# Performance work log

Hardware: AMD Instinct MI355X
Metric: run time of the kernel (lower is better)

Reference implementation:

```python
import jax, jax.numpy as jnp
import numpy as np

B, S, D = 32, 2048, 64

def setup_inputs() -> dict:
    key = jax.random.key(0)
    kq, kk, kv = jax.random.split(key, 3)
    return {
        "query": jax.random.normal(kq, (B, S, D), dtype=jnp.float32),
        "key": jax.random.normal(kk, (B, S, D), dtype=jnp.float32),
        "value": jax.random.normal(kv, (B, S, D), dtype=jnp.float32),
    }

def reference(query, key, value):
    # scores: [B, S, S] = Q @ K^T / sqrt(d_k)  (scale=True)
    d_k = key.shape[-1]
    scores = jnp.einsum("bqd,bkd->bqk", query, key) / jnp.sqrt(jnp.asarray(d_k, query.dtype))
    # exp + normalize over last dim == softmax (no mask, dropout in eval mode)
    attn = jax.nn.softmax(scores, axis=-1)
    # context: [B, S, D] = attn @ V
    context = jnp.einsum("bqk,bkd->bqd", attn, value)
    return context
```

## Files before the change

kernel.cpp:

```cpp
#include <hip/hip_runtime.h>
#include <hip/hip_bf16.h>

#define B_   32
#define S_   2048
#define D_   64
#define KVB  64
#define NT   (S_/KVB)
#define NW   4
#define QW   64
#define QB   (NW*QW)

typedef __attribute__((ext_vector_type(8)))  __bf16 bf16x8;
typedef __attribute__((ext_vector_type(4)))  __bf16 bf16x4;
typedef __attribute__((ext_vector_type(16))) float  f32x16;

__device__ __forceinline__ float fexp2(float x) {
#if __has_builtin(__builtin_amdgcn_exp2f)
    return __builtin_amdgcn_exp2f(x);
#else
    return exp2f(x);
#endif
}

__device__ __forceinline__ unsigned pk2(float a, float b) {
    unsigned r;
    asm("v_cvt_pk_bf16_f32 %0, %1, %2" : "=v"(r) : "v"(a), "v"(b));
    return r;
}

__device__ __forceinline__ void pl32swap(unsigned &a, unsigned &b) {
#if __has_builtin(__builtin_amdgcn_permlane32_swap)
    auto r = __builtin_amdgcn_permlane32_swap(a, b, false, false);
    a = (unsigned)r[0]; b = (unsigned)r[1];
#else
    unsigned pa = (unsigned)__shfl_xor((int)a, 32);
    unsigned pb = (unsigned)__shfl_xor((int)b, 32);
    bool hi = (threadIdx.x & 32) != 0;
    unsigned na = hi ? pb : a;
    unsigned nb = hi ? b  : pa;
    a = na; b = nb;
#endif
}

__device__ __forceinline__ f32x16 z16() {
    f32x16 z;
    #pragma unroll
    for (int i = 0; i < 16; ++i) z[i] = 0.f;
    return z;
}

struct PBpair { bf16x8 a, b; };

__device__ __forceinline__ PBpair pack2(const f32x16 ps) {
    unsigned y0 = pk2(ps[0],  ps[1]);
    unsigned y1 = pk2(ps[2],  ps[3]);
    unsigned y2 = pk2(ps[4],  ps[5]);
    unsigned y3 = pk2(ps[6],  ps[7]);
    pl32swap(y0, y2); pl32swap(y1, y3);
    unsigned z0 = pk2(ps[8],  ps[9]);
    unsigned z1 = pk2(ps[10], ps[11]);
    unsigned z2 = pk2(ps[12], ps[13]);
    unsigned z3 = pk2(ps[14], ps[15]);
    pl32swap(z0, z2); pl32swap(z1, z3);
    union { unsigned u[4]; bf16x8 v; } pa, pbu;
    pa.u[0]=y0;  pa.u[1]=y1;  pa.u[2]=y2;  pa.u[3]=y3;
    pbu.u[0]=z0; pbu.u[1]=z1; pbu.u[2]=z2; pbu.u[3]=z3;
    PBpair r; r.a = pa.v; r.b = pbu.v; return r;
}

__global__ __launch_bounds__(256, 1)
void attn_fwd(const float* __restrict__ Q, const float* __restrict__ K,
              const float* __restrict__ V, float* __restrict__ Out)
{
    __shared__ __align__(16) __bf16 Kt[3][KVB * D_];
    __shared__ __align__(16) __bf16 Vt[3][D_ * KVB];

    const int tid  = threadIdx.x;
    const int w    = tid >> 6;
    const int lane = tid & 63;
    const int l31  = lane & 31;
    const int hi   = lane >> 5;

    const int bid = blockIdx.x;
    const int swz = ((bid & 7) << 5) | (bid >> 3);
    const int b   = swz >> 3;
    const int q0  = (swz & 7) * QB;

    const float SCL = 0.18033688011112042f;
    bf16x8 qfA[4], qfB[4];
    #pragma unroll
    for (int qt = 0; qt < 2; ++qt) {
        const float* qp = Q + ((size_t)(b*S_ + q0 + w*QW + qt*32 + l31))*D_ + hi*8;
        #pragma unroll
        for (int ks = 0; ks < 4; ++ks) {
            float4 f0 = *reinterpret_cast<const float4*>(qp + ks*16);
            float4 f1 = *reinterpret_cast<const float4*>(qp + ks*16 + 4);
            bf16x8 a;
            a[0]=(__bf16)(f0.x*SCL); a[1]=(__bf16)(f0.y*SCL);
            a[2]=(__bf16)(f0.z*SCL); a[3]=(__bf16)(f0.w*SCL);
            a[4]=(__bf16)(f1.x*SCL); a[5]=(__bf16)(f1.y*SCL);
            a[6]=(__bf16)(f1.z*SCL); a[7]=(__bf16)(f1.w*SCL);
            if (qt == 0) qfA[ks]=a; else qfB[ks]=a;
        }
    }

    int offK[4], offV[4];
    #pragma unroll
    for (int i = 0; i < 4; ++i) {
        offK[i] = l31*128 + (((i*32) + hi*16) ^ ((l31 & 7) << 4));
        offV[i] = l31*128 + (((i*32) + hi*16) ^ (((l31 >> 1) & 7) << 4));
    }

    const float* kg = K + (size_t)b*S_*D_;
    const float* vg = V + (size_t)b*S_*D_;

    const int krow0 = tid >> 4;
    const int kcol  = (tid & 15) * 4;
    const int kwr0  = krow0*128 + ((kcol*2) ^ ((krow0 & 7) << 4));

    const int kv0 = (tid >> 4) * 2;
    const int db  = (tid & 15) * 2;
    int vwr[4];
    #pragma unroll
    for (int j = 0; j < 4; ++j) {
        int d = db + (j >> 1)*32 + (j & 1);
        vwr[j] = d*128 + ((kv0*2) ^ (((d >> 1) & 7) << 4));
    }

#define STAGE_LOAD(T)                                                              \
    {   const float* kt_ = kg + (size_t)(T)*KVB*D_;                                \
        const float* vt_ = vg + (size_t)(T)*KVB*D_;                                \
        ka0 = *reinterpret_cast<const float4*>(kt_ + krow0*64 + kcol);             \
        ka1 = *reinterpret_cast<const float4*>(kt_ + (krow0+16)*64 + kcol);        \
        ka2 = *reinterpret_cast<const float4*>(kt_ + (krow0+32)*64 + kcol);        \
        ka3 = *reinterpret_cast<const float4*>(kt_ + (krow0+48)*64 + kcol);        \
        v0a = *reinterpret_cast<const float2*>(vt_ + kv0*64 + db);                 \
        v1a = *reinterpret_cast<const float2*>(vt_ + (kv0+1)*64 + db);             \
        v0b = *reinterpret_cast<const float2*>(vt_ + kv0*64 + db + 32);            \
        v1b = *reinterpret_cast<const float2*>(vt_ + (kv0+1)*64 + db + 32);        \
        v2a = *reinterpret_cast<const float2*>(vt_ + (kv0+32)*64 + db);            \
        v3a = *reinterpret_cast<const float2*>(vt_ + (kv0+33)*64 + db);            \
        v2b = *reinterpret_cast<const float2*>(vt_ + (kv0+32)*64 + db + 32);       \
        v3b = *reinterpret_cast<const float2*>(vt_ + (kv0+33)*64 + db + 32);       }

#define STAGE_WRITE(BUF)                                                           \
    {   char* kw = (char*)&Kt[(BUF)][0];                                           \
        char* vw = (char*)&Vt[(BUF)][0];                                           \
        bf16x4 h0 = {(__bf16)ka0.x,(__bf16)ka0.y,(__bf16)ka0.z,(__bf16)ka0.w};     \
        bf16x4 h1 = {(__bf16)ka1.x,(__bf16)ka1.y,(__bf16)ka1.z,(__bf16)ka1.w};     \
        bf16x4 h2 = {(__bf16)ka2.x,(__bf16)ka2.y,(__bf16)ka2.z,(__bf16)ka2.w};     \
        bf16x4 h3 = {(__bf16)ka3.x,(__bf16)ka3.y,(__bf16)ka3.z,(__bf16)ka3.w};     \
        *reinterpret_cast<bf16x4*>(kw + kwr0)        = h0;                         \
        *reinterpret_cast<bf16x4*>(kw + kwr0 + 2048) = h1;                         \
        *reinterpret_cast<bf16x4*>(kw + kwr0 + 4096) = h2;                         \
        *reinterpret_cast<bf16x4*>(kw + kwr0 + 6144) = h3;                         \
        *reinterpret_cast<unsigned*>(vw + vwr[0])        = pk2(v0a.x, v1a.x);      \
        *reinterpret_cast<unsigned*>(vw + vwr[1])        = pk2(v0a.y, v1a.y);      \
        *reinterpret_cast<unsigned*>(vw + vwr[2])        = pk2(v0b.x, v1b.x);      \
        *reinterpret_cast<unsigned*>(vw + vwr[3])        = pk2(v0b.y, v1b.y);      \
        *reinterpret_cast<unsigned*>(vw + (vwr[0] ^ 64)) = pk2(v2a.x, v3a.x);      \
        *reinterpret_cast<unsigned*>(vw + (vwr[1] ^ 64)) = pk2(v2a.y, v3a.y);      \
        *reinterpret_cast<unsigned*>(vw + (vwr[2] ^ 64)) = pk2(v2b.x, v3b.x);      \
        *reinterpret_cast<unsigned*>(vw + (vwr[3] ^ 64)) = pk2(v2b.y, v3b.y);      }

    float4 ka0, ka1, ka2, ka3;
    float2 v0a, v1a, v0b, v1b, v2a, v3a, v2b, v3b;

    STAGE_LOAD(0)
    STAGE_WRITE(0)
    __syncthreads();

    float lA = 0.f, lB = 0.f;
    f32x16 oA0 = z16(), oA1 = z16(), oB0 = z16(), oB1 = z16();
    PBpair pA01, pA23, pB01, pB23;

#define SOFTMAX_PACK()                                                             \
    {   _Pragma("unroll")                                                          \
        for (int r = 0; r < 16; ++r) sA0[r] = fexp2(sA0[r]);                       \
        _Pragma("unroll")                                                          \
        for (int r = 0; r < 16; ++r) sA1[r] = fexp2(sA1[r]);                       \
        _Pragma("unroll")                                                          \
        for (int r = 0; r < 16; ++r) sB0[r] = fexp2(sB0[r]);                       \
        _Pragma("unroll")                                                          \
        for (int r = 0; r < 16; ++r) sB1[r] = fexp2(sB1[r]);                       \
        float tA[16], tB[16];                                                      \
        _Pragma("unroll")                                                          \
        for (int i = 0; i < 16; ++i) { tA[i] = sA0[i] + sA1[i];                    \
                                       tB[i] = sB0[i] + sB1[i]; }                  \
        _Pragma("unroll")                                                          \
        for (int st = 8; st > 0; st >>= 1)                                         \
            _Pragma("unroll")                                                      \
            for (int i = 0; i < st; ++i) { tA[i] += tA[i+st]; tB[i] += tB[i+st]; } \
        lA += tA[0] + __shfl_xor(tA[0], 32);                                       \
        lB += tB[0] + __shfl_xor(tB[0], 32);                                       \
        pA01 = pack2(sA0); pA23 = pack2(sA1);                                      \
        pB01 = pack2(sB0); pB23 = pack2(sB1);                                      }

#define QK_BOTH(KBUF)                                                              \
    {   const char* kbuf = (const char*)&Kt[(KBUF)][0];                            \
        __builtin_amdgcn_s_setprio(1);                                             \
        _Pragma("unroll")                                                          \
        for (int ks = 0; ks < 4; ++ks) {                                           \
            bf16x8 k0 = *reinterpret_cast<const bf16x8*>(kbuf + offK[ks]);         \
            bf16x8 k1 = *reinterpret_cast<const bf16x8*>(kbuf + offK[ks] + 4096);  \
            sA0 = __builtin_amdgcn_mfma_f32_32x32x16_bf16(k0, qfA[ks], sA0, 0,0,0);\
            sB0 = __builtin_amdgcn_mfma_f32_32x32x16_bf16(k0, qfB[ks], sB0, 0,0,0);\
            sA1 = __builtin_amdgcn_mfma_f32_32x32x16_bf16(k1, qfA[ks], sA1, 0,0,0);\
            sB1 = __builtin_amdgcn_mfma_f32_32x32x16_bf16(k1, qfB[ks], sB1, 0,0,0);\
        }                                                                          \
        __builtin_amdgcn_s_setprio(0);                                             }

#define PV_BOTH(VBUF)                                                              \
    {   const char* vbuf = (const char*)&Vt[(VBUF)][0];                            \
        __builtin_amdgcn_s_setprio(1);                                             \
        _Pragma("unroll")                                                          \
        for (int c = 0; c < 4; ++c) {                                              \
            bf16x8 pa = (c==0)?pA01.a:(c==1)?pA01.b:(c==2)?pA23.a:pA23.b;          \
            bf16x8 pb = (c==0)?pB01.a:(c==1)?pB01.b:(c==2)?pB23.a:pB23.b;          \
            bf16x8 v0 = *reinterpret_cast<const bf16x8*>(vbuf + offV[c]);          \
            bf16x8 v1 = *reinterpret_cast<const bf16x8*>(vbuf + offV[c] + 4096);   \
            oA0 = __builtin_amdgcn_mfma_f32_32x32x16_bf16(v0, pa, oA0, 0,0,0);     \
            oB0 = __builtin_amdgcn_mfma_f32_32x32x16_bf16(v0, pb, oB0, 0,0,0);     \
            oA1 = __builtin_amdgcn_mfma_f32_32x32x16_bf16(v1, pa, oA1, 0,0,0);     \
            oB1 = __builtin_amdgcn_mfma_f32_32x32x16_bf16(v1, pb, oB1, 0,0,0);     \
        }                                                                          \
        __builtin_amdgcn_s_setprio(0);                                             }

    {
        STAGE_LOAD(1)
        f32x16 sA0 = z16(), sA1 = z16(), sB0 = z16(), sB1 = z16();
        QK_BOTH(0)
        SOFTMAX_PACK()
        STAGE_WRITE(1)
        __syncthreads();
    }

    for (int t = 1; t < NT; ++t) {
        const int cur = t % 3;
        const int prv = (t-1) % 3;
        const int nxt = (t+1) % 3;
        const int tn  = (t+1 < NT) ? (t+1) : t;
        STAGE_LOAD(tn)

        f32x16 sA0 = z16(), sA1 = z16(), sB0 = z16(), sB1 = z16();
        QK_BOTH(cur)
        PV_BOTH(prv)
        SOFTMAX_PACK()

        STAGE_WRITE(nxt)
        __syncthreads();
    }

    PV_BOTH((NT-1) % 3)

    {
        float invl = 1.0f / lA;
        float* orow = Out + ((size_t)(b*S_ + q0 + w*QW + l31))*D_;
        #pragma unroll
        for (int rr = 0; rr < 4; ++rr) {
            float4 res;
            res.x = oA0[rr*4+0]*invl; res.y = oA0[rr*4+1]*invl;
            res.z = oA0[rr*4+2]*invl; res.w = oA0[rr*4+3]*invl;
            *reinterpret_cast<float4*>(orow + rr*8 + hi*4) = res;
        }
        #pragma unroll
        for (int rr = 0; rr < 4; ++rr) {
            float4 res;
            res.x = oA1[rr*4+0]*invl; res.y = oA1[rr*4+1]*invl;
            res.z = oA1[rr*4+2]*invl; res.w = oA1[rr*4+3]*invl;
            *reinterpret_cast<float4*>(orow + 32 + rr*8 + hi*4) = res;
        }
    }
    {
        float invl = 1.0f / lB;
        float* orow = Out + ((size_t)(b*S_ + q0 + w*QW + 32 + l31))*D_;
        #pragma unroll
        for (int rr = 0; rr < 4; ++rr) {
            float4 res;
            res.x = oB0[rr*4+0]*invl; res.y = oB0[rr*4+1]*invl;
            res.z = oB0[rr*4+2]*invl; res.w = oB0[rr*4+3]*invl;
            *reinterpret_cast<float4*>(orow + rr*8 + hi*4) = res;
        }
        #pragma unroll
        for (int rr = 0; rr < 4; ++rr) {
            float4 res;
            res.x = oB1[rr*4+0]*invl; res.y = oB1[rr*4+1]*invl;
            res.z = oB1[rr*4+2]*invl; res.w = oB1[rr*4+3]*invl;
            *reinterpret_cast<float4*>(orow + 32 + rr*8 + hi*4) = res;
        }
    }
}

extern "C" void kernel_launch(void* const* d_in, const int* in_sizes, int n_in,
                              void* d_out, int out_size, void* d_ws, size_t ws_size,
                              hipStream_t stream) {
    const float* Q = (const float*)d_in[0];
    const float* K = (const float*)d_in[1];
    const float* V = (const float*)d_in[2];
    float* O = (float*)d_out;
    attn_fwd<<<dim3(B_ * (S_ / QB)), dim3(256), 0, stream>>>(Q, K, V, O);
}
```

Baseline: 62.46 us.

## Split KV sequence across two wave groups per block and merge partial outputs

Doubles the block to 512 threads (8 waves), where two groups of four waves each process half of every 128-row KV step for the same 256 queries, so the loop runs half as many iterations per wave. Partial O accumulators and row sums from group 1 are merged into group 0 through shared memory, reusing the K buffer, before normalization. The first QK MFMA now takes a zero accumulator instead of a zero-initialized register. The change raises per-CU wave count and latency hiding, at the cost of double the LDS staging, extra syncs and an LDS reduction epilogue.

```diff
diff --git a/kernel.cpp b/kernel.cpp
--- a/kernel.cpp
+++ b/kernel.cpp
@@ -5,10 +5,8 @@
 #define S_   2048
 #define D_   64
 #define KVB  64
-#define NT   (S_/KVB)
-#define NW   4
-#define QW   64
-#define QB   (NW*QW)
+#define NP   16
+#define QB   256
 
 typedef __attribute__((ext_vector_type(8)))  __bf16 bf16x8;
 typedef __attribute__((ext_vector_type(4)))  __bf16 bf16x4;
@@ -40,13 +38,6 @@
     unsigned nb = hi ? b  : pa;
     a = na; b = nb;
 #endif
-}
-
-__device__ __forceinline__ f32x16 z16() {
-    f32x16 z;
-    #pragma unroll
-    for (int i = 0; i < 16; ++i) z[i] = 0.f;
-    return z;
 }
 
 struct PBpair { bf16x8 a, b; };
@@ -68,18 +59,20 @@
     PBpair r; r.a = pa.v; r.b = pbu.v; return r;
 }
 
-__global__ __launch_bounds__(256, 1)
+__global__ __launch_bounds__(512, 2)
 void attn_fwd(const float* __restrict__ Q, const float* __restrict__ K,
               const float* __restrict__ V, float* __restrict__ Out)
 {
-    __shared__ __align__(16) __bf16 Kt[3][KVB * D_];
-    __shared__ __align__(16) __bf16 Vt[3][D_ * KVB];
+    __shared__ __align__(16) __bf16 Kt[3][2][KVB * D_];
+    __shared__ __align__(16) __bf16 Vt[3][2][D_ * KVB];
 
     const int tid  = threadIdx.x;
     const int w    = tid >> 6;
     const int lane = tid & 63;
     const int l31  = lane & 31;
     const int hi   = lane >> 5;
+    const int g2   = w >> 2;
+    const int qsub = w & 3;
 
     const int bid = blockIdx.x;
     const int swz = ((bid & 7) << 5) | (bid >> 3);
@@ -90,7 +83,7 @@
     bf16x8 qfA[4], qfB[4];
     #pragma unroll
     for (int qt = 0; qt < 2; ++qt) {
-        const float* qp = Q + ((size_t)(b*S_ + q0 + w*QW + qt*32 + l31))*D_ + hi*8;
+        const float* qp = Q + ((size_t)(b*S_ + q0 + qsub*64 + qt*32 + l31))*D_ + hi*8;
         #pragma unroll
         for (int ks = 0; ks < 4; ++ks) {
             float4 f0 = *reinterpret_cast<const float4*>(qp + ks*16);
@@ -114,12 +107,15 @@
     const float* kg = K + (size_t)b*S_*D_;
     const float* vg = V + (size_t)b*S_*D_;
 
-    const int krow0 = tid >> 4;
-    const int kcol  = (tid & 15) * 4;
+    const int ts   = tid >> 8;
+    const int t256 = tid & 255;
+
+    const int krow0 = t256 >> 4;
+    const int kcol  = (t256 & 15) * 4;
     const int kwr0  = krow0*128 + ((kcol*2) ^ ((krow0 & 7) << 4));
 
-    const int kv0 = (tid >> 4) * 2;
-    const int db  = (tid & 15) * 2;
+    const int kv0 = (t256 >> 4) * 2;
+    const int db  = (t256 & 15) * 2;
     int vwr[4];
     #pragma unroll
     for (int j = 0; j < 4; ++j) {
@@ -127,9 +123,9 @@
         vwr[j] = d*128 + ((kv0*2) ^ (((d >> 1) & 7) << 4));
     }
 
-#define STAGE_LOAD(T)                                                              \
-    {   const float* kt_ = kg + (size_t)(T)*KVB*D_;                                \
-        const float* vt_ = vg + (size_t)(T)*KVB*D_;                                \
+#define STAGE_LOAD(P)                                                              \
+    {   const float* kt_ = kg + ((size_t)(P)*128 + ts*64)*64;                      \
+        const float* vt_ = vg + ((size_t)(P)*128 + ts*64)*64;                      \
         ka0 = *reinterpret_cast<const float4*>(kt_ + krow0*64 + kcol);             \
         ka1 = *reinterpret_cast<const float4*>(kt_ + (krow0+16)*64 + kcol);        \
         ka2 = *reinterpret_cast<const float4*>(kt_ + (krow0+32)*64 + kcol);        \
@@ -144,8 +140,8 @@
         v3b = *reinterpret_cast<const float2*>(vt_ + (kv0+33)*64 + db + 32);       }
 
 #define STAGE_WRITE(BUF)                                                           \
-    {   char* kw = (char*)&Kt[(BUF)][0];                                           \
-        char* vw = (char*)&Vt[(BUF)][0];                                           \
+    {   char* kw = (char*)&Kt[(BUF)][ts][0];                                       \
+        char* vw = (char*)&Vt[(BUF)][ts][0];                                       \
         bf16x4 h0 = {(__bf16)ka0.x,(__bf16)ka0.y,(__bf16)ka0.z,(__bf16)ka0.w};     \
         bf16x4 h1 = {(__bf16)ka1.x,(__bf16)ka1.y,(__bf16)ka1.z,(__bf16)ka1.w};     \
         bf16x4 h2 = {(__bf16)ka2.x,(__bf16)ka2.y,(__bf16)ka2.z,(__bf16)ka2.w};     \
@@ -166,41 +162,26 @@
     float4 ka0, ka1, ka2, ka3;
     float2 v0a, v1a, v0b, v1b, v2a, v3a, v2b, v3b;
 
-    STAGE_LOAD(0)
-    STAGE_WRITE(0)
-    __syncthreads();
+    f32x16 ZV;
+    #pragma unroll
+    for (int i = 0; i < 16; ++i) ZV[i] = 0.f;
 
     float lA = 0.f, lB = 0.f;
-    f32x16 oA0 = z16(), oA1 = z16(), oB0 = z16(), oB1 = z16();
+    f32x16 oA0 = ZV, oA1 = ZV, oB0 = ZV, oB1 = ZV;
     PBpair pA01, pA23, pB01, pB23;
 
-#define SOFTMAX_PACK()                                                             \
-    {   _Pragma("unroll")                                                          \
-        for (int r = 0; r < 16; ++r) sA0[r] = fexp2(sA0[r]);                       \
-        _Pragma("unroll")                                                          \
-        for (int r = 0; r < 16; ++r) sA1[r] = fexp2(sA1[r]);                       \
-        _Pragma("unroll")                                                          \
-        for (int r = 0; r < 16; ++r) sB0[r] = fexp2(sB0[r]);                       \
-        _Pragma("unroll")                                                          \
-        for (int r = 0; r < 16; ++r) sB1[r] = fexp2(sB1[r]);                       \
-        float tA[16], tB[16];                                                      \
-        _Pragma("unroll")                                                          \
-        for (int i = 0; i < 16; ++i) { tA[i] = sA0[i] + sA1[i];                    \
-                                       tB[i] = sB0[i] + sB1[i]; }                  \
-        _Pragma("unroll")                                                          \
-        for (int st = 8; st > 0; st >>= 1)                                         \
-            _Pragma("unroll")                                                      \
-            for (int i = 0; i < st; ++i) { tA[i] += tA[i+st]; tB[i] += tB[i+st]; } \
-        lA += tA[0] + __shfl_xor(tA[0], 32);                                       \
-        lB += tB[0] + __shfl_xor(tB[0], 32);                                       \
-        pA01 = pack2(sA0); pA23 = pack2(sA1);                                      \
-        pB01 = pack2(sB0); pB23 = pack2(sB1);                                      }
-
 #define QK_BOTH(KBUF)                                                              \
-    {   const char* kbuf = (const char*)&Kt[(KBUF)][0];                            \
+    {   const char* kbuf = (const char*)&Kt[(KBUF)][g2][0];                        \
         __builtin_amdgcn_s_setprio(1);                                             \
-        _Pragma("unroll")                                                          \
-        for (int ks = 0; ks < 4; ++ks) {                                           \
+        {   bf16x8 k0 = *reinterpret_cast<const bf16x8*>(kbuf + offK[0]);          \
+            bf16x8 k1 = *reinterpret_cast<const bf16x8*>(kbuf + offK[0] + 4096);   \
+            sA0 = __builtin_amdgcn_mfma_f32_32x32x16_bf16(k0, qfA[0], ZV, 0,0,0);  \
+            sB0 = __builtin_amdgcn_mfma_f32_32x32x16_bf16(k0, qfB[0], ZV, 0,0,0);  \
+            sA1 = __builtin_amdgcn_mfma_f32_32x32x16_bf16(k1, qfA[0], ZV, 0,0,0);  \
+            sB1 = __builtin_amdgcn_mfma_f32_32x32x16_bf16(k1, qfB[0], ZV, 0,0,0);  \
+        }                                                                          \
+        _Pragma("unroll")                                                          \
+        for (int ks = 1; ks < 4; ++ks) {                                           \
             bf16x8 k0 = *reinterpret_cast<const bf16x8*>(kbuf + offK[ks]);         \
             bf16x8 k1 = *reinterpret_cast<const bf16x8*>(kbuf + offK[ks] + 4096);  \
             sA0 = __builtin_amdgcn_mfma_f32_32x32x16_bf16(k0, qfA[ks], sA0, 0,0,0);\
@@ -211,7 +192,7 @@
         __builtin_amdgcn_s_setprio(0);                                             }
 
 #define PV_BOTH(VBUF)                                                              \
-    {   const char* vbuf = (const char*)&Vt[(VBUF)][0];                            \
+    {   const char* vbuf = (const char*)&Vt[(VBUF)][g2][0];                        \
         __builtin_amdgcn_s_setprio(1);                                             \
         _Pragma("unroll")                                                          \
         for (int c = 0; c < 4; ++c) {                                              \
@@ -226,23 +207,48 @@
         }                                                                          \
         __builtin_amdgcn_s_setprio(0);                                             }
 
+#define SOFTMAX_PACK()                                                             \
+    {   _Pragma("unroll")                                                          \
+        for (int r = 0; r < 16; ++r) sA0[r] = fexp2(sA0[r]);                       \
+        _Pragma("unroll")                                                          \
+        for (int r = 0; r < 16; ++r) sA1[r] = fexp2(sA1[r]);                       \
+        _Pragma("unroll")                                                          \
+        for (int r = 0; r < 16; ++r) sB0[r] = fexp2(sB0[r]);                       \
+        _Pragma("unroll")                                                          \
+        for (int r = 0; r < 16; ++r) sB1[r] = fexp2(sB1[r]);                       \
+        float tA[16], tB[16];                                                      \
+        _Pragma("unroll")                                                          \
+        for (int i = 0; i < 16; ++i) { tA[i] = sA0[i] + sA1[i];                    \
+                                       tB[i] = sB0[i] + sB1[i]; }                  \
+        _Pragma("unroll")                                                          \
+        for (int st = 8; st > 0; st >>= 1)                                         \
+            _Pragma("unroll")                                                      \
+            for (int i = 0; i < st; ++i) { tA[i] += tA[i+st]; tB[i] += tB[i+st]; } \
+        lA += tA[0] + __shfl_xor(tA[0], 32);                                       \
+        lB += tB[0] + __shfl_xor(tB[0], 32);                                       \
+        pA01 = pack2(sA0); pA23 = pack2(sA1);                                      \
+        pB01 = pack2(sB0); pB23 = pack2(sB1);                                      }
+
+    STAGE_LOAD(0)
+    STAGE_WRITE(0)
+    __syncthreads();
+
     {
         STAGE_LOAD(1)
-        f32x16 sA0 = z16(), sA1 = z16(), sB0 = z16(), sB1 = z16();
+        f32x16 sA0, sA1, sB0, sB1;
         QK_BOTH(0)
         SOFTMAX_PACK()
         STAGE_WRITE(1)
         __syncthreads();
     }
 
-    for (int t = 1; t < NT; ++t) {
-        const int cur = t % 3;
-        const int prv = (t-1) % 3;
-        const int nxt = (t+1) % 3;
-        const int tn  = (t+1 < NT) ? (t+1) : t;
-        STAGE_LOAD(tn)
-
-        f32x16 sA0 = z16(), sA1 = z16(), sB0 = z16(), sB1 = z16();
+    for (int p = 1; p < NP; ++p) {
+        const int cur = p % 3;
+        const int prv = (p-1) % 3;
+        const int nxt = (p+1) % 3;
+        STAGE_LOAD(p+1 < NP ? p+1 : p)
+
+        f32x16 sA0, sA1, sB0, sB1;
         QK_BOTH(cur)
         PV_BOTH(prv)
         SOFTMAX_PACK()
@@ -251,42 +257,72 @@
         __syncthreads();
     }
 
-    PV_BOTH((NT-1) % 3)
-
-    {
-        float invl = 1.0f / lA;
-        float* orow = Out + ((size_t)(b*S_ + q0 + w*QW + l31))*D_;
+    PV_BOTH((NP-1) % 3)
+
+    float* M = reinterpret_cast<float*>(&Kt[0][0][0]);
+    const int mqA = qsub*64 + l31;
+    const int mqB = mqA + 32;
+    float invlA = 0.f, invlB = 0.f;
+
+    if (g2 == 1) {
+        #pragma unroll
+        for (int rr = 0; rr < 4; ++rr)
+            #pragma unroll
+            for (int j = 0; j < 4; ++j) {
+                M[mqA*33 + rr*8 + hi*4 + j] = oA0[rr*4+j];
+                M[mqB*33 + rr*8 + hi*4 + j] = oB0[rr*4+j];
+            }
+        if (hi == 0) { M[mqA*33 + 32] = lA; M[mqB*33 + 32] = lB; }
+    }
+    __syncthreads();
+    if (g2 == 0) {
+        lA += M[mqA*33 + 32];
+        lB += M[mqB*33 + 32];
+        invlA = 1.0f / lA; invlB = 1.0f / lB;
+        float* orowA = Out + ((size_t)(b*S_ + q0 + mqA))*D_;
+        float* orowB = Out + ((size_t)(b*S_ + q0 + mqB))*D_;
         #pragma unroll
         for (int rr = 0; rr < 4; ++rr) {
-            float4 res;
-            res.x = oA0[rr*4+0]*invl; res.y = oA0[rr*4+1]*invl;
-            res.z = oA0[rr*4+2]*invl; res.w = oA0[rr*4+3]*invl;
-            *reinterpret_cast<float4*>(orow + rr*8 + hi*4) = res;
+            float4 ra, rb;
+            ra.x = (oA0[rr*4+0] + M[mqA*33 + rr*8 + hi*4 + 0]) * invlA;
+            ra.y = (oA0[rr*4+1] + M[mqA*33 + rr*8 + hi*4 + 1]) * invlA;
+            ra.z = (oA0[rr*4+2] + M[mqA*33 + rr*8 + hi*4 + 2]) * invlA;
+            ra.w = (oA0[rr*4+3] + M[mqA*33 + rr*8 + hi*4 + 3]) * invlA;
+            rb.x = (oB0[rr*4+0] + M[mqB*33 + rr*8 + hi*4 + 0]) * invlB;
+            rb.y = (oB0[rr*4+1] + M[mqB*33 + rr*8 + hi*4 + 1]) * invlB;
+            rb.z = (oB0[rr*4+2] + M[mqB*33 + rr*8 + hi*4 + 2]) * invlB;
+            rb.w = (oB0[rr*4+3] + M[mqB*33 + rr*8 + hi*4 + 3]) * invlB;
+            *reinterpret_cast<float4*>(orowA + rr*8 + hi*4) = ra;
+            *reinterpret_cast<float4*>(orowB + rr*8 + hi*4) = rb;
         }
+    }
+    __syncthreads();
+    if (g2 == 1) {
+        #pragma unroll
+        for (int rr = 0; rr < 4; ++rr)
+            #pragma unroll
+            for (int j = 0; j < 4; ++j) {
+                M[mqA*33 + rr*8 + hi*4 + j] = oA1[rr*4+j];
+                M[mqB*33 + rr*8 + hi*4 + j] = oB1[rr*4+j];
+            }
+    }
+    __syncthreads();
+    if (g2 == 0) {
+        float* orowA = Out + ((size_t)(b*S_ + q0 + mqA))*D_ + 32;
+        float* orowB = Out + ((size_t)(b*S_ + q0 + mqB))*D_ + 32;
         #pragma unroll
         for (int rr = 0; rr < 4; ++rr) {
-            float4 res;
-            res.x = oA1[rr*4+0]*invl; res.y = oA1[rr*4+1]*invl;
-            res.z = oA1[rr*4+2]*invl; res.w = oA1[rr*4+3]*invl;
-            *reinterpret_cast<float4*>(orow + 32 + rr*8 + hi*4) = res;
-        }
-    }
-    {
-        float invl = 1.0f / lB;
-        float* orow = Out + ((size_t)(b*S_ + q0 + w*QW + 32 + l31))*D_;
-        #pragma unroll
-        for (int rr = 0; rr < 4; ++rr) {
-            float4 res;
-            res.x = oB0[rr*4+0]*invl; res.y = oB0[rr*4+1]*invl;
-            res.z = oB0[rr*4+2]*invl; res.w = oB0[rr*4+3]*invl;
-            *reinterpret_cast<float4*>(orow + rr*8 + hi*4) = res;
-        }
-        #pragma unroll
-        for (int rr = 0; rr < 4; ++rr) {
-            float4 res;
-            res.x = oB1[rr*4+0]*invl; res.y = oB1[rr*4+1]*invl;
-            res.z = oB1[rr*4+2]*invl; res.w = oB1[rr*4+3]*invl;
-            *reinterpret_cast<float4*>(orow + 32 + rr*8 + hi*4) = res;
+            float4 ra, rb;
+            ra.x = (oA1[rr*4+0] + M[mqA*33 + rr*8 + hi*4 + 0]) * invlA;
+            ra.y = (oA1[rr*4+1] + M[mqA*33 + rr*8 + hi*4 + 1]) * invlA;
+            ra.z = (oA1[rr*4+2] + M[mqA*33 + rr*8 + hi*4 + 2]) * invlA;
+            ra.w = (oA1[rr*4+3] + M[mqA*33 + rr*8 + hi*4 + 3]) * invlA;
+            rb.x = (oB1[rr*4+0] + M[mqB*33 + rr*8 + hi*4 + 0]) * invlB;
+            rb.y = (oB1[rr*4+1] + M[mqB*33 + rr*8 + hi*4 + 1]) * invlB;
+            rb.z = (oB1[rr*4+2] + M[mqB*33 + rr*8 + hi*4 + 2]) * invlB;
+            rb.w = (oB1[rr*4+3] + M[mqB*33 + rr*8 + hi*4 + 3]) * invlB;
+            *reinterpret_cast<float4*>(orowA + rr*8 + hi*4) = ra;
+            *reinterpret_cast<float4*>(orowB + rr*8 + hi*4) = rb;
         }
     }
 }
@@ -298,5 +334,5 @@
     const float* K = (const float*)d_in[1];
     const float* V = (const float*)d_in[2];
     float* O = (float*)d_out;
-    attn_fwd<<<dim3(B_ * (S_ / QB)), dim3(256), 0, stream>>>(Q, K, V, O);
-}
+    attn_fwd<<<dim3(B_ * (S_ / QB)), dim3(512), 0, stream>>>(Q, K, V, O);
+}
```

After: 75.91 us. +21.5%, slower.
